# Kernel optimization log

Hardware: AMD Instinct MI355X
Metric: run time of the kernel (lower is better)

## Reference

```python
import jax, jax.numpy as jnp
import numpy as np

HIDDEN = 4096
N_EXPERTS = 128
TOP_K = 8
N_GROUP = 1
TOPK_GROUP = 1
NORM_TOPK_PROB = True
ROUTED_SCALING = 1.0


def setup_inputs() -> dict:
    key = jax.random.key(0)
    k1, k2, k3 = jax.random.split(key, 3)
    hidden_states = jax.random.normal(k1, (4, 4096, HIDDEN), dtype=jnp.float32)
    weight = jax.random.normal(k2, (N_EXPERTS, HIDDEN), dtype=jnp.float32) * 0.02
    e_score_correction_bias = jax.random.normal(k3, (N_EXPERTS,), dtype=jnp.float32) * 0.02
    return {
        "hidden_states": hidden_states,
        "weight": weight,
        "e_score_correction_bias": e_score_correction_bias,
    }


def reference(hidden_states, weight, e_score_correction_bias):
    # flatten tokens: [T, H]
    h = hidden_states.reshape(-1, HIDDEN).astype(jnp.float32)
    # router logits -> sigmoid scores  [T, E]
    logits = jnp.einsum("th,eh->te", h, weight.astype(jnp.float32))
    scores = jax.nn.sigmoid(logits)
    scores_for_choice = scores + e_score_correction_bias[None, :]
    T = scores.shape[0]
    # group scores: sum of top-2 (bias-corrected) scores within each group  [T, G]
    grouped = scores_for_choice.reshape(T, N_GROUP, N_EXPERTS // N_GROUP)
    group_scores = jax.lax.top_k(grouped, 2)[0].sum(axis=-1)
    # select top groups, build expert mask  [T, E]
    group_idx = jax.lax.top_k(group_scores, TOPK_GROUP)[1]          # [T, topk_group]
    group_mask = jnp.zeros((T, N_GROUP), scores.dtype).at[
        jnp.arange(T)[:, None], group_idx].set(1.0)
    score_mask = jnp.repeat(group_mask, N_EXPERTS // N_GROUP, axis=1)
    masked_scores = jnp.where(score_mask > 0, scores_for_choice, 0.0)
    # final top-k experts over masked scores; weights gathered from raw scores
    topk_indices = jax.lax.top_k(masked_scores, TOP_K)[1]           # [T, top_k]
    topk_weights = jnp.take_along_axis(scores, topk_indices, axis=1)
    if NORM_TOPK_PROB:
        denom = topk_weights.sum(axis=-1, keepdims=True) + 1e-20
        topk_weights = topk_weights / denom
    topk_weights = topk_weights * ROUTED_SCALING
    return topk_indices, topk_weights
```

## Files before the change

### kernel.cpp

```cpp
#include <hip/hip_runtime.h>
#include <math.h>

#define HIDDEN 4096
#define NEXP   128
#define TOPK   8
#define BM     64
#define BKC    64
#define NCHUNK (HIDDEN / BKC)
#define SS     132

#define AH    0
#define AMID  4096
#define ALO   8192
#define BH    12288
#define BMID  20480
#define BLO   28672
#define SMEM_USHORT 36864

typedef __attribute__((ext_vector_type(8))) short short8;
typedef __attribute__((ext_vector_type(4))) float f32x4;

struct Split3 { uint4 h, m, l; };

__device__ __forceinline__ unsigned pack2(unsigned a, unsigned b) {
  return (a >> 16) | (b & 0xFFFF0000u);
}

__device__ __forceinline__ Split3 split8(float4 a, float4 b) {
  float x[8] = {a.x, a.y, a.z, a.w, b.x, b.y, b.z, b.w};
  unsigned h[8], m[8], l[8];
#pragma unroll
  for (int j = 0; j < 8; ++j) {
    unsigned u  = __float_as_uint(x[j]);
    unsigned hb = (u + 0x8000u) & 0xFFFF0000u;
    float rh    = x[j] - __uint_as_float(hb);
    unsigned um = __float_as_uint(rh);
    unsigned mb = (um + 0x8000u) & 0xFFFF0000u;
    float rm    = rh - __uint_as_float(mb);
    h[j] = hb; m[j] = mb; l[j] = __float_as_uint(rm);
  }
  Split3 s;
  s.h = make_uint4(pack2(h[0],h[1]), pack2(h[2],h[3]), pack2(h[4],h[5]), pack2(h[6],h[7]));
  s.m = make_uint4(pack2(m[0],m[1]), pack2(m[2],m[3]), pack2(m[4],m[5]), pack2(m[6],m[7]));
  s.l = make_uint4(pack2(l[0],l[1]), pack2(l[2],l[3]), pack2(l[4],l[6]^l[6]^l[6]), 0);
  s.l = make_uint4(pack2(l[0],l[1]), pack2(l[2],l[3]), pack2(l[4],l[5]), pack2(l[6],l[7]));
  return s;
}

__global__ __launch_bounds__(512, 2) void router_kernel(
    const float* __restrict__ h,
    const float* __restrict__ w,
    const float* __restrict__ bias,
    float* __restrict__ out,
    int T)
{
  __shared__ __align__(16) ushort smem_u[SMEM_USHORT];
  const int tid  = threadIdx.x;
  const int row0 = blockIdx.x * BM;

  const int wid  = tid >> 6;
  const int wn   = wid & 3;
  const int wk   = wid >> 2;
  const int lane = tid & 63;
  const int lrow = lane & 15;
  const int lk   = lane >> 4;

  const int sr = tid >> 3;
  const int sk = tid & 7;
  const float* gA  = h + (size_t)(row0 + sr) * HIDDEN + sk * 8;
  const float* gB0 = w + (size_t)sr * HIDDEN + sk * 8;
  const float* gB1 = gB0 + (size_t)64 * HIDDEN;

  const int sixA  = (sr * 64 + sk * 8) ^ ((sr & 7) << 3);
  const int rB1   = 64 + sr;
  const int sixB1 = (rB1 * 64 + sk * 8) ^ ((rB1 & 7) << 3);

  f32x4 acc[4][2];
#pragma unroll
  for (int i = 0; i < 4; ++i)
#pragma unroll
    for (int j = 0; j < 2; ++j) acc[i][j] = (f32x4){0.f, 0.f, 0.f, 0.f};

  float4 pa0  = *(const float4*)(gA);
  float4 pa1  = *(const float4*)(gA + 4);
  float4 pb00 = *(const float4*)(gB0);
  float4 pb01 = *(const float4*)(gB0 + 4);
  float4 pb10 = *(const float4*)(gB1);
  float4 pb11 = *(const float4*)(gB1 + 4);

  for (int c = 0; c < NCHUNK; ++c) {
    __syncthreads();
    {
      Split3 s = split8(pa0, pa1);
      *(uint4*)(smem_u + AH   + sixA) = s.h;
      *(uint4*)(smem_u + AMID + sixA) = s.m;
      *(uint4*)(smem_u + ALO  + sixA) = s.l;
    }
    {
      Split3 s = split8(pb00, pb01);
      *(uint4*)(smem_u + BH   + sixA) = s.h;
      *(uint4*)(smem_u + BMID + sixA) = s.m;
      *(uint4*)(smem_u + BLO  + sixA) = s.l;
    }
    {
      Split3 s = split8(pb10, pb11);
      *(uint4*)(smem_u + BH   + sixB1) = s.h;
      *(uint4*)(smem_u + BMID + sixB1) = s.m;
      *(uint4*)(smem_u + BLO  + sixB1) = s.l;
    }
    if (c + 1 < NCHUNK) {
      const int ko = (c + 1) * BKC;
      pa0  = *(const float4*)(gA + ko);
      pa1  = *(const float4*)(gA + ko + 4);
      pb00 = *(const float4*)(gB0 + ko);
      pb01 = *(const float4*)(gB0 + ko + 4);
      pb10 = *(const float4*)(gB1 + ko);
      pb11 = *(const float4*)(gB1 + ko + 4);
    }
    __syncthreads();

    short8 a_h[4], a_m[4], a_l[4];
#pragma unroll
    for (int mi = 0; mi < 4; ++mi) {
      const int r  = mi * 16 + lrow;
      const int ix = (r * 64 + wk * 32 + lk * 8) ^ ((r & 7) << 3);
      a_h[mi] = *(const short8*)(smem_u + AH   + ix);
      a_m[mi] = *(const short8*)(smem_u + AMID + ix);
      a_l[mi] = *(const short8*)(smem_u + ALO  + ix);
    }
    short8 b_h[2], b_m[2], b_l[2];
#pragma unroll
    for (int ni = 0; ni < 2; ++ni) {
      const int e  = wn * 32 + ni * 16 + lrow;
      const int ix = (e * 64 + wk * 32 + lk * 8) ^ ((e & 7) << 3);
      b_h[ni] = *(const short8*)(smem_u + BH   + ix);
      b_m[ni] = *(const short8*)(smem_u + BMID + ix);
      b_l[ni] = *(const short8*)(smem_u + BLO  + ix);
    }
#pragma unroll
    for (int mi = 0; mi < 4; ++mi)
#pragma unroll
      for (int ni = 0; ni < 2; ++ni) {
        f32x4 cc = acc[mi][ni];
        cc = __builtin_amdgcn_mfma_f32_16x16x32_bf16(a_h[mi], b_h[ni], cc, 0, 0, 0);
        cc = __builtin_amdgcn_mfma_f32_16x16x32_bf16(a_h[mi], b_m[ni], cc, 0, 0, 0);
        cc = __builtin_amdgcn_mfma_f32_16x16x32_bf16(a_m[mi], b_h[ni], cc, 0, 0, 0);
        cc = __builtin_amdgcn_mfma_f32_16x16x32_bf16(a_h[mi], b_l[ni], cc, 0, 0, 0);
        cc = __builtin_amdgcn_mfma_f32_16x16x32_bf16(a_l[mi], b_h[ni], cc, 0, 0, 0);
        cc = __builtin_amdgcn_mfma_f32_16x16x32_bf16(a_m[mi], b_m[ni], cc, 0, 0, 0);
        acc[mi][ni] = cc;
      }
  }

  __syncthreads();
  float* Ss = (float*)smem_u;
  if (wk == 1) {
#pragma unroll
    for (int mi = 0; mi < 4; ++mi)
#pragma unroll
      for (int ni = 0; ni < 2; ++ni)
#pragma unroll
        for (int j = 0; j < 4; ++j)
          Ss[(mi * 16 + lk * 4 + j) * SS + wn * 32 + ni * 16 + lrow] = acc[mi][ni][j];
  }
  __syncthreads();
  if (wk == 0) {
#pragma unroll
    for (int mi = 0; mi < 4; ++mi)
#pragma unroll
      for (int ni = 0; ni < 2; ++ni)
#pragma unroll
        for (int j = 0; j < 4; ++j) {
          const int ixs = (mi * 16 + lk * 4 + j) * SS + wn * 32 + ni * 16 + lrow;
          Ss[ixs] += acc[mi][ni][j];
        }
  }
  __syncthreads();

  const float bb0 = bias[lane];
  const float bb1 = bias[lane + 64];

  for (int t = wid; t < BM; t += 8) {
    const float lg0 = Ss[t * SS + lane];
    const float lg1 = Ss[t * SS + 64 + lane];
    const float s0 = 1.0f / (1.0f + expf(-lg0));
    const float s1 = 1.0f / (1.0f + expf(-lg1));
    float c0 = s0 + bb0;
    float c1 = s1 + bb1;

    int   sel_i[TOPK];
    float sel_r[TOPK];
    float rsum = 0.0f;
#pragma unroll
    for (int j = 0; j < TOPK; ++j) {
      const bool take0 = (c0 >= c1);
      float v  = take0 ? c0 : c1;
      float rr = take0 ? s0 : s1;
      int   ii = take0 ? lane : lane + 64;
#pragma unroll
      for (int off = 32; off > 0; off >>= 1) {
        const float ov  = __shfl_xor(v, off, 64);
        const float orr = __shfl_xor(rr, off, 64);
        const int   oi  = __shfl_xor(ii, off, 64);
        if (ov > v || (ov == v && oi < ii)) { v = ov; rr = orr; ii = oi; }
      }
      sel_i[j] = ii;
      sel_r[j] = rr;
      rsum += rr;
      if (ii == lane)      c0 = -__builtin_inff();
      if (ii == lane + 64) c1 = -__builtin_inff();
    }
    if (lane == 0) {
      const float inv = 1.0f / (rsum + 1e-20f);
      const size_t tok = (size_t)(row0 + t);
#pragma unroll
      for (int j = 0; j < TOPK; ++j) {
        out[tok * TOPK + j]                    = (float)sel_i[j];
        out[(size_t)T * TOPK + tok * TOPK + j] = sel_r[j] * inv;
      }
    }
  }
}

extern "C" void kernel_launch(void* const* d_in, const int* in_sizes, int n_in,
                              void* d_out, int out_size, void* d_ws, size_t ws_size,
                              hipStream_t stream) {
  const float* h    = (const float*)d_in[0];
  const float* w    = (const float*)d_in[1];
  const float* bias = (const float*)d_in[2];
  float* out = (float*)d_out;
  const int T = in_sizes[0] / HIDDEN;

  dim3 grid(T / BM);
  dim3 block(512);
  hipLaunchKernelGGL(router_kernel, grid, block, 0, stream, h, w, bias, out, T);
}
```

Baseline: 427.8 us.

## Pre-split router weights into MFMA-fragment layout and stream B from global

A new pre-pass kernel splits the fp32 router weight into three bf16 parts (hi/mid/lo) and stores them in the exact per-lane MFMA fragment order in the workspace. The main kernel then loads B fragments directly from global/L2 instead of re-splitting the weight through shared memory in every block. Only A is staged, in a double-buffered LDS tile, which removes one barrier per chunk. The token tile shrinks from 64 to 32 rows and the occupancy hint rises, trading more blocks and more repeated weight reads from L2 for less LDS traffic and less split arithmetic per block.

```diff
diff --git a/kernel.cpp b/kernel.cpp
--- a/kernel.cpp
+++ b/kernel.cpp
@@ -4,28 +4,21 @@
 #define HIDDEN 4096
 #define NEXP   128
 #define TOPK   8
-#define BM     64
+#define BM     32
 #define BKC    64
 #define NCHUNK (HIDDEN / BKC)
 #define SS     132
 
-#define AH    0
-#define AMID  4096
-#define ALO   8192
-#define BH    12288
-#define BMID  20480
-#define BLO   28672
-#define SMEM_USHORT 36864
+#define SMEM_USHORT 12288
 
 typedef __attribute__((ext_vector_type(8))) short short8;
 typedef __attribute__((ext_vector_type(4))) float f32x4;
 
-struct Split3 { uint4 h, m, l; };
-
 __device__ __forceinline__ unsigned pack2(unsigned a, unsigned b) {
   return (a >> 16) | (b & 0xFFFF0000u);
 }
 
+struct Split3 { uint4 h, m, l; };
 __device__ __forceinline__ Split3 split8(float4 a, float4 b) {
   float x[8] = {a.x, a.y, a.z, a.w, b.x, b.y, b.z, b.w};
   unsigned h[8], m[8], l[8];
@@ -42,15 +35,54 @@
   Split3 s;
   s.h = make_uint4(pack2(h[0],h[1]), pack2(h[2],h[3]), pack2(h[4],h[5]), pack2(h[6],h[7]));
   s.m = make_uint4(pack2(m[0],m[1]), pack2(m[2],m[3]), pack2(m[4],m[5]), pack2(m[6],m[7]));
-  s.l = make_uint4(pack2(l[0],l[1]), pack2(l[2],l[3]), pack2(l[4],l[6]^l[6]^l[6]), 0);
   s.l = make_uint4(pack2(l[0],l[1]), pack2(l[2],l[3]), pack2(l[4],l[5]), pack2(l[6],l[7]));
   return s;
 }
 
-__global__ __launch_bounds__(512, 2) void router_kernel(
-    const float* __restrict__ h,
-    const float* __restrict__ w,
-    const float* __restrict__ bias,
+struct Split3x4 { uint2 h, m, l; };
+__device__ __forceinline__ Split3x4 split4(float4 a) {
+  float x[4] = {a.x, a.y, a.z, a.w};
+  unsigned h[4], m[4], l[4];
+#pragma unroll
+  for (int j = 0; j < 4; ++j) {
+    unsigned u  = __float_as_uint(x[j]);
+    unsigned hb = (u + 0x8000u) & 0xFFFF0000u;
+    float rh    = x[j] - __uint_as_float(hb);
+    unsigned um = __float_as_uint(rh);
+    unsigned mb = (um + 0x8000u) & 0xFFFF0000u;
+    float rm    = rh - __uint_as_float(mb);
+    h[j] = hb; m[j] = mb; l[j] = __float_as_uint(rm);
+  }
+  Split3x4 s;
+  s.h = make_uint2(pack2(h[0],h[1]), pack2(h[2],h[3]));
+  s.m = make_uint2(pack2(m[0],m[1]), pack2(m[2],m[3]));
+  s.l = make_uint2(pack2(l[0],l[1]), pack2(l[2],l[3]));
+  return s;
+}
+
+__global__ __launch_bounds__(256) void pack_w_kernel(
+    const float* __restrict__ w, ushort* __restrict__ wp)
+{
+  const int g    = blockIdx.x * 256 + threadIdx.x;
+  const int lane = g & 63;
+  const int fid  = g >> 6;
+  const int et   = fid >> 7;
+  const int kc   = fid & 127;
+  const int e    = et * 16 + (lane & 15);
+  const int k0   = kc * 32 + (lane >> 4) * 8;
+  const float4 x0 = *(const float4*)(w + (size_t)e * HIDDEN + k0);
+  const float4 x1 = *(const float4*)(w + (size_t)e * HIDDEN + k0 + 4);
+  Split3 s = split8(x0, x1);
+  uint4* dst = (uint4*)wp + (size_t)fid * 3 * 64;
+  dst[0 * 64 + lane] = s.h;
+  dst[1 * 64 + lane] = s.m;
+  dst[2 * 64 + lane] = s.l;
+}
+
+__global__ __launch_bounds__(512, 4) void router_kernel(
+    const float*  __restrict__ h,
+    const ushort* __restrict__ wp,
+    const float*  __restrict__ bias,
     float* __restrict__ out,
     int T)
 {
@@ -65,89 +97,61 @@
   const int lrow = lane & 15;
   const int lk   = lane >> 4;
 
-  const int sr = tid >> 3;
-  const int sk = tid & 7;
-  const float* gA  = h + (size_t)(row0 + sr) * HIDDEN + sk * 8;
-  const float* gB0 = w + (size_t)sr * HIDDEN + sk * 8;
-  const float* gB1 = gB0 + (size_t)64 * HIDDEN;
-
-  const int sixA  = (sr * 64 + sk * 8) ^ ((sr & 7) << 3);
-  const int rB1   = 64 + sr;
-  const int sixB1 = (rB1 * 64 + sk * 8) ^ ((rB1 & 7) << 3);
-
-  f32x4 acc[4][2];
-#pragma unroll
-  for (int i = 0; i < 4; ++i)
+  const int sr = tid >> 4;
+  const int sk = tid & 15;
+  const float* gA = h + (size_t)(row0 + sr) * HIDDEN + sk * 4;
+  const int six   = (sr * 64 + sk * 4) ^ ((sr & 7) << 3);
+
+  f32x4 acc[2][2];
+#pragma unroll
+  for (int i = 0; i < 2; ++i)
 #pragma unroll
     for (int j = 0; j < 2; ++j) acc[i][j] = (f32x4){0.f, 0.f, 0.f, 0.f};
 
-  float4 pa0  = *(const float4*)(gA);
-  float4 pa1  = *(const float4*)(gA + 4);
-  float4 pb00 = *(const float4*)(gB0);
-  float4 pb01 = *(const float4*)(gB0 + 4);
-  float4 pb10 = *(const float4*)(gB1);
-  float4 pb11 = *(const float4*)(gB1 + 4);
+  float4 pa = *(const float4*)(gA);
 
   for (int c = 0; c < NCHUNK; ++c) {
+    const int kc = c * 2 + wk;
+    short8 bf[2][3];
+#pragma unroll
+    for (int ni = 0; ni < 2; ++ni) {
+      const size_t fb = (size_t)((wn * 2 + ni) * 128 + kc) * 1536 + lane * 8;
+#pragma unroll
+      for (int s = 0; s < 3; ++s)
+        bf[ni][s] = *(const short8*)(wp + fb + s * 512);
+    }
+
+    const int b    = c & 1;
+    const int abuf = b * 6144;
+    {
+      Split3x4 s = split4(pa);
+      *(uint2*)(smem_u + abuf +    0 + six) = s.h;
+      *(uint2*)(smem_u + abuf + 2048 + six) = s.m;
+      *(uint2*)(smem_u + abuf + 4096 + six) = s.l;
+    }
+    if (c + 1 < NCHUNK) pa = *(const float4*)(gA + (c + 1) * BKC);
     __syncthreads();
-    {
-      Split3 s = split8(pa0, pa1);
-      *(uint4*)(smem_u + AH   + sixA) = s.h;
-      *(uint4*)(smem_u + AMID + sixA) = s.m;
-      *(uint4*)(smem_u + ALO  + sixA) = s.l;
-    }
-    {
-      Split3 s = split8(pb00, pb01);
-      *(uint4*)(smem_u + BH   + sixA) = s.h;
-      *(uint4*)(smem_u + BMID + sixA) = s.m;
-      *(uint4*)(smem_u + BLO  + sixA) = s.l;
-    }
-    {
-      Split3 s = split8(pb10, pb11);
-      *(uint4*)(smem_u + BH   + sixB1) = s.h;
-      *(uint4*)(smem_u + BMID + sixB1) = s.m;
-      *(uint4*)(smem_u + BLO  + sixB1) = s.l;
-    }
-    if (c + 1 < NCHUNK) {
-      const int ko = (c + 1) * BKC;
-      pa0  = *(const float4*)(gA + ko);
-      pa1  = *(const float4*)(gA + ko + 4);
-      pb00 = *(const float4*)(gB0 + ko);
-      pb01 = *(const float4*)(gB0 + ko + 4);
-      pb10 = *(const float4*)(gB1 + ko);
-      pb11 = *(const float4*)(gB1 + ko + 4);
-    }
-    __syncthreads();
-
-    short8 a_h[4], a_m[4], a_l[4];
-#pragma unroll
-    for (int mi = 0; mi < 4; ++mi) {
+
+    short8 af[2][3];
+#pragma unroll
+    for (int mi = 0; mi < 2; ++mi) {
       const int r  = mi * 16 + lrow;
       const int ix = (r * 64 + wk * 32 + lk * 8) ^ ((r & 7) << 3);
-      a_h[mi] = *(const short8*)(smem_u + AH   + ix);
-      a_m[mi] = *(const short8*)(smem_u + AMID + ix);
-      a_l[mi] = *(const short8*)(smem_u + ALO  + ix);
-    }
-    short8 b_h[2], b_m[2], b_l[2];
-#pragma unroll
-    for (int ni = 0; ni < 2; ++ni) {
-      const int e  = wn * 32 + ni * 16 + lrow;
-      const int ix = (e * 64 + wk * 32 + lk * 8) ^ ((e & 7) << 3);
-      b_h[ni] = *(const short8*)(smem_u + BH   + ix);
-      b_m[ni] = *(const short8*)(smem_u + BMID + ix);
-      b_l[ni] = *(const short8*)(smem_u + BLO  + ix);
-    }
-#pragma unroll
-    for (int mi = 0; mi < 4; ++mi)
+      af[mi][0] = *(const short8*)(smem_u + abuf +    0 + ix);
+      af[mi][1] = *(const short8*)(smem_u + abuf + 2048 + ix);
+      af[mi][2] = *(const short8*)(smem_u + abuf + 4096 + ix);
+    }
+#pragma unroll
+    for (int mi = 0; mi < 2; ++mi)
 #pragma unroll
       for (int ni = 0; ni < 2; ++ni) {
         f32x4 cc = acc[mi][ni];
-        cc = __builtin_amdgcn_mfma_f32_16x16x32_bf16(a_h[mi], b_h[ni], cc, 0, 0, 0);
-        cc = __builtin_amdgcn_mfma_f32_16x16x32_bf16(a_h[mi], b_m[ni], cc, 0, 0, 0);
-        cc = __builtin_amdgcn_mfma_f32_16x16x32_bf16(a_m[mi], b_h[ni], cc, 0, 0, 0);
-        cc = __builtin_amdgcn_mfma_f32_16x16x32_bf16(a_h[mi], b_l[ni], cc, 0, 0, 0);
-        cc = __builtin_amdgcn_mfma_f32_16x16x32_bf16(a_l[mi], b_h[ni], cc, 0, 0, 0);
-        cc = __builtin_amdgcn_mfma_f32_16x16x32_bf16(a_m[mi], b_m[ni], cc, 0, 0, 0);
+        cc = __builtin_amdgcn_mfma_f32_16x16x32_bf16(af[mi][0], bf[ni][0], cc, 0, 0, 0);
+        cc = __builtin_amdgcn_mfma_f32_16x16x32_bf16(af[mi][0], bf[ni][1], cc, 0, 0, 0);
+        cc = __builtin_amdgcn_mfma_f32_16x16x32_bf16(af[mi][1], bf[ni][0], cc, 0, 0, 0);
+        cc = __builtin_amdgcn_mfma_f32_16x16x32_bf16(af[mi][0], bf[ni][2], cc, 0, 0, 0);
+        cc = __builtin_amdgcn_mfma_f32_16x16x32_bf16(af[mi][2], bf[ni][0], cc, 0, 0, 0);
+        cc = __builtin_amdgcn_mfma_f32_16x16x32_bf16(af[mi][1], bf[ni][1], cc, 0, 0, 0);
         acc[mi][ni] = cc;
       }
   }
@@ -156,7 +160,7 @@
   float* Ss = (float*)smem_u;
   if (wk == 1) {
 #pragma unroll
-    for (int mi = 0; mi < 4; ++mi)
+    for (int mi = 0; mi < 2; ++mi)
 #pragma unroll
       for (int ni = 0; ni < 2; ++ni)
 #pragma unroll
@@ -166,7 +170,7 @@
   __syncthreads();
   if (wk == 0) {
 #pragma unroll
-    for (int mi = 0; mi < 4; ++mi)
+    for (int mi = 0; mi < 2; ++mi)
 #pragma unroll
       for (int ni = 0; ni < 2; ++ni)
 #pragma unroll
@@ -229,9 +233,12 @@
   const float* w    = (const float*)d_in[1];
   const float* bias = (const float*)d_in[2];
   float* out = (float*)d_out;
+  ushort* wp = (ushort*)d_ws;
   const int T = in_sizes[0] / HIDDEN;
+
+  hipLaunchKernelGGL(pack_w_kernel, dim3(256), dim3(256), 0, stream, w, wp);
 
   dim3 grid(T / BM);
   dim3 block(512);
-  hipLaunchKernelGGL(router_kernel, grid, block, 0, stream, h, w, bias, out, T);
-}
+  hipLaunchKernelGGL(router_kernel, grid, block, 0, stream, h, wp, bias, out, T);
+}
```

New measurement: 448.7 us. +4.9%, slower.
